# Optimization experiments

Hardware: AMD Instinct MI355X
Metric: run time of the kernel (lower is better)

Reference implementation:

```python
import jax, jax.numpy as jnp
import numpy as np

THETA = 128.0


def _make_Q(d, units):
    # Q[n,m] = (2n+1)/sqrt(d) if n > m and (n+m) odd, else 0 (fixed, non-trainable)
    n = np.arange(d)[:, None]
    m = np.arange(units)[None, :]
    Q = np.where((n > m) & (((n + m) % 2) == 1), (2 * n + 1) / np.sqrt(d), 0.0)
    return jnp.asarray(Q, dtype=jnp.float32)


def setup_inputs() -> dict:
    key = jax.random.key(0)
    k1, k2, k3, k4 = jax.random.split(key, 4)
    B_, T, Din, d, units = 16, 4096, 128, 256, 256
    x = jax.random.normal(k1, (B_, T, Din), dtype=jnp.float32)
    A = jax.random.normal(k2, (d, d), dtype=jnp.float32) / np.sqrt(d)
    Bm = jax.random.normal(k3, (Din, d), dtype=jnp.float32) / np.sqrt(Din)
    W_mix = jax.random.normal(k4, (units, units), dtype=jnp.float32) / np.sqrt(units)
    b_mix = jnp.zeros((units,), dtype=jnp.float32)
    return {"x": x, "A": A, "B": Bm, "W_mix": W_mix, "b_mix": b_mix}


def reference(x, A, B, W_mix, b_mix):
    d = A.shape[0]
    units = W_mix.shape[0]
    Q = _make_Q(d, units)
    QW = Q @ W_mix  # fuse fixed projection with dense kernel: (d, units)
    alpha = 1.0 - 1.0 / THETA
    beta = 1.0 / THETA
    # precompute input projection for all steps: (T, batch, d)
    xB = jnp.einsum('bti,id->tbd', x, B)

    def step(state, xBt):
        new_state = alpha * state + beta * (state @ A + xBt)
        y = jnp.tanh(new_state @ QW + b_mix)
        return new_state, y

    s0 = jnp.zeros((x.shape[0], d), dtype=x.dtype)
    _, ys = jax.lax.scan(step, s0, xB)  # ys: (T, batch, units)
    return jnp.transpose(ys, (1, 0, 2))
```

## Files before the change

### kernel.cpp

```cpp
#include <hip/hip_runtime.h>
#include <math.h>

constexpr int T_   = 4096;
constexpr int NB   = 16;
constexpr int D_   = 256;
constexpr int DIN  = 128;
constexpr int U_   = 256;
constexpr int L1   = 8;
constexpr int C1   = T_ / L1;
constexpr float ALPHA_ = 1.0f - 1.0f / 128.0f;
constexpr float BETA_  = 1.0f / 128.0f;
constexpr int SD   = NB * D_;
constexpr int MS   = D_ * D_;
constexpr int TLP  = D_ + 4;
constexpr int XLP  = DIN + 4;

using short8  = __attribute__((ext_vector_type(8))) short;
using float4v = __attribute__((ext_vector_type(4))) float;

__device__ __forceinline__ unsigned short bf16_rne(float x) {
  const unsigned b = __float_as_uint(x);
  const unsigned r = ((b >> 16) & 1u) + 0x7FFFu;
  return (unsigned short)((b + r) >> 16);
}
__device__ __forceinline__ float bf16_f(unsigned short h) {
  return __uint_as_float(((unsigned)h) << 16);
}

__device__ __forceinline__ void split2(float e0, float e1, unsigned& hd, unsigned& ld) {
  const unsigned b0 = __float_as_uint(e0), b1 = __float_as_uint(e1);
  const unsigned h0 = b0 & 0xFFFF0000u, h1 = b1 & 0xFFFF0000u;
  const float l0 = e0 - __uint_as_float(h0);
  const float l1 = e1 - __uint_as_float(h1);
  hd = (h0 >> 16) | h1;
  ld = (__float_as_uint(l0) >> 16) | (__float_as_uint(l1) & 0xFFFF0000u);
}

__device__ __forceinline__ void unpack8(uint4 a, uint4 b, short8& hi, short8& lo) {
  union { short8 s; unsigned u[4]; } H, L;
  const unsigned d[8] = {a.x, a.y, a.z, a.w, b.x, b.y, b.z, b.w};
#pragma unroll
  for (int i = 0; i < 4; ++i) {
    H.u[i] = (d[2 * i] >> 16) | (d[2 * i + 1] & 0xFFFF0000u);
    L.u[i] = (d[2 * i] & 0xFFFFu) | (d[2 * i + 1] << 16);
  }
  hi = H.s; lo = L.s;
}

__device__ __forceinline__ void mm_row(const float* __restrict__ Am,
                                       const float* __restrict__ Bm,
                                       float* __restrict__ Dm,
                                       int i, int tid, float* srow) {
  srow[tid] = Am[i * D_ + tid];
  __syncthreads();
  float a0 = 0.f, a1 = 0.f, a2 = 0.f, a3 = 0.f;
#pragma unroll 8
  for (int k = 0; k < D_; k += 4) {
    a0 = fmaf(srow[k + 0], Bm[(k + 0) * D_ + tid], a0);
    a1 = fmaf(srow[k + 1], Bm[(k + 1) * D_ + tid], a1);
    a2 = fmaf(srow[k + 2], Bm[(k + 2) * D_ + tid], a2);
    a3 = fmaf(srow[k + 3], Bm[(k + 3) * D_ + tid], a3);
  }
  Dm[i * D_ + tid] = (a0 + a1) + (a2 + a3);
  __syncthreads();
}

__global__ __launch_bounds__(256) void k_prep(const float* __restrict__ A,
                                              const float* __restrict__ W,
                                              float* __restrict__ Meff,
                                              float* __restrict__ QW) {
  const int bid = blockIdx.x, tid = threadIdx.x;
  if (bid < D_) {
    float v = BETA_ * A[bid * D_ + tid];
    if (bid == tid) v += ALPHA_;
    Meff[bid * D_ + tid] = v;
    return;
  }
  __shared__ float wch[32 * D_];
  float se = 0.f, so = 0.f;
  for (int ch = 0; ch < D_ / 32; ++ch) {
    __syncthreads();
    for (int idx = tid; idx < 32 * D_; idx += 256)
      wch[idx] = W[ch * 32 * D_ + idx];
    __syncthreads();
#pragma unroll
    for (int r = 0; r < 32; ++r) {
      const int n = ch * 32 + r;
      const float sum = (n & 1) ? se : so;
      QW[n * U_ + tid] = sum * ((float)(2 * n + 1) / 16.0f);
      const float wv = wch[r * D_ + tid];
      if (n & 1) so += wv; else se += wv;
    }
  }
}

__global__ __launch_bounds__(256) void k_pw(const float* __restrict__ Am,
                                            const float* __restrict__ Bbase,
                                            float* __restrict__ Dbase) {
  __shared__ float srow[D_];
  const int q = blockIdx.x >> 8, row = blockIdx.x & 255;
  mm_row(Am, Bbase + (size_t)q * MS, Dbase + (size_t)q * MS, row, threadIdx.x, srow);
}

__global__ __launch_bounds__(256) void k_pwr(const float* __restrict__ Abase,
                                             const float* __restrict__ Bm,
                                             float* __restrict__ Dbase) {
  __shared__ float srow[D_];
  const int q = blockIdx.x >> 8, row = blockIdx.x & 255;
  mm_row(Abase + (size_t)q * MS, Bm, Dbase + (size_t)q * MS, row, threadIdx.x, srow);
}

__global__ __launch_bounds__(256) void k_packA(const float* __restrict__ A,
                                               const float* __restrict__ Bm,
                                               unsigned short* __restrict__ Mf,
                                               unsigned short* __restrict__ Bmf) {
  const int bid = blockIdx.x, tid = threadIdx.x;
  const int lane = tid & 63, nb0 = tid >> 6;
  const int quad = lane >> 4, m16 = lane & 15;
  if (bid < 8) {
    const int ks = bid;
    for (int nb = nb0; nb < 16; nb += 4) {
      const size_t fo = ((size_t)(nb * 8 + ks) * 64 + lane) * 8;
#pragma unroll
      for (int jj = 0; jj < 8; ++jj) {
        const int k = ks * 32 + quad * 8 + jj;
        const int n = nb * 16 + m16;
        const float v = BETA_ * A[k * D_ + n];
        const unsigned short h = bf16_rne(v);
        Mf[fo + jj] = h;
        Mf[MS + fo + jj] = bf16_rne(v - bf16_f(h));
      }
    }
  } else {
    const int ks = bid - 8;
    unsigned short* dh = Bmf;
    unsigned short* dl = Bmf + (MS / 2);
    for (int nb = nb0; nb < 16; nb += 4) {
      const size_t fo = ((size_t)(nb * 4 + ks) * 64 + lane) * 8;
#pragma unroll
      for (int jj = 0; jj < 8; ++jj) {
        const int k = ks * 32 + quad * 8 + jj;
        const int n = nb * 16 + m16;
        const float v = BETA_ * Bm[k * D_ + n];
        const unsigned short h = bf16_rne(v);
        dh[fo + jj] = h;
        dl[fo + jj] = bf16_rne(v - bf16_f(h));
      }
    }
  }
}

__global__ __launch_bounds__(256) void k_packB(const float* __restrict__ R,
                                               const float* __restrict__ QWm,
                                               const float* __restrict__ M8,
                                               unsigned short* __restrict__ Bf,
                                               unsigned short* __restrict__ Pf0) {
  const int bid = blockIdx.x;
  const int mat = bid >> 3, ks = bid & 7;
  const float* X = (mat < 8) ? (R + (size_t)mat * MS) : (mat == 8 ? QWm : M8);
  unsigned short* dh = (mat < 9) ? (Bf + (size_t)mat * (2 * MS)) : Pf0;
  unsigned short* dl = dh + MS;
  const int tid = threadIdx.x, lane = tid & 63, nb0 = tid >> 6;
  const int quad = lane >> 4, m16 = lane & 15;
  for (int nb = nb0; nb < 16; nb += 4) {
    const size_t fo = ((size_t)(nb * 8 + ks) * 64 + lane) * 8;
#pragma unroll
    for (int jj = 0; jj < 8; ++jj) {
      const int k = ks * 32 + quad * 8 + jj;
      const int n = nb * 16 + m16;
      const float xv = X[k * D_ + n];
      const unsigned short h = bf16_rne(xv);
      dh[fo + jj] = h;
      dl[fo + jj] = bf16_rne(xv - bf16_f(h));
    }
  }
}

__global__ __launch_bounds__(256, 2) void k_passA(
    const float* __restrict__ x, const unsigned short* __restrict__ Bmf,
    const unsigned short* __restrict__ Mf,
    unsigned short* __restrict__ Shi, unsigned short* __restrict__ Slo,
    float* __restrict__ Ends) {
  __shared__ __align__(16) float xls[NB][XLP];
  __shared__ __align__(16) unsigned tls[NB][TLP];
  const int c = blockIdx.x, tid = threadIdx.x;
  const int w = tid >> 6, lane = tid & 63;
  const int m16 = lane & 15, q = lane >> 4;
  const int xrow = tid >> 4, xi0 = (tid & 15) * 8;

  float4v sC[4];
#pragma unroll
  for (int nt = 0; nt < 4; ++nt) sC[nt] = (float4v){0.f, 0.f, 0.f, 0.f};

  for (int j = 0; j < L1; ++j) {
    const int t = c * L1 + j;
    __syncthreads();
    {
      const float* xr = x + ((size_t)xrow * T_ + t) * DIN + xi0;
      const float4 v0 = *(const float4*)(xr);
      const float4 v1 = *(const float4*)(xr + 4);
      *(float4*)(&xls[xrow][xi0]) = v0;
      *(float4*)(&xls[xrow][xi0 + 4]) = v1;
    }
    if (j > 0) {
#pragma unroll
      for (int nt = 0; nt < 4; ++nt) {
        const int n = (w * 4 + nt) * 16 + m16;
#pragma unroll
        for (int r = 0; r < 4; ++r) {
          const float sv = sC[nt][r];
          const unsigned hb = __float_as_uint(sv) & 0xFFFF0000u;
          const float lo = sv - __uint_as_float(hb);
          tls[4 * q + r][n] = hb | (__float_as_uint(lo) >> 16);
        }
      }
    }
    __syncthreads();
    float4v acc[4];
#pragma unroll
    for (int nt = 0; nt < 4; ++nt) {
      acc[nt][0] = ALPHA_ * sC[nt][0];
      acc[nt][1] = ALPHA_ * sC[nt][1];
      acc[nt][2] = ALPHA_ * sC[nt][2];
      acc[nt][3] = ALPHA_ * sC[nt][3];
    }
#pragma unroll
    for (int ks = 0; ks < 4; ++ks) {
      float xv[8];
      *(float4*)(xv)     = *(const float4*)(&xls[m16][32 * ks + 8 * q]);
      *(float4*)(xv + 4) = *(const float4*)(&xls[m16][32 * ks + 8 * q + 4]);
      union { short8 s; unsigned u[4]; } XH, XL;
#pragma unroll
      for (int p = 0; p < 4; ++p) split2(xv[2 * p], xv[2 * p + 1], XH.u[p], XL.u[p]);
#pragma unroll
      for (int nt = 0; nt < 4; ++nt) {
        const size_t fo = ((size_t)((w * 4 + nt) * 4 + ks) * 64 + lane) * 8;
        const short8 bh = *(const short8*)(Bmf + fo);
        const short8 bl = *(const short8*)(Bmf + (MS / 2) + fo);
        acc[nt] = __builtin_amdgcn_mfma_f32_16x16x32_bf16(XH.s, bh, acc[nt], 0, 0, 0);
        acc[nt] = __builtin_amdgcn_mfma_f32_16x16x32_bf16(XH.s, bl, acc[nt], 0, 0, 0);
        acc[nt] = __builtin_amdgcn_mfma_f32_16x16x32_bf16(XL.s, bh, acc[nt], 0, 0, 0);
      }
    }
    if (j > 0) {
#pragma unroll
      for (int ks = 0; ks < 8; ++ks) {
        const uint4 p0 = *(const uint4*)(&tls[m16][32 * ks + 8 * q]);
        const uint4 p1 = *(const uint4*)(&tls[m16][32 * ks + 8 * q + 4]);
        short8 sh, sl; unpack8(p0, p1, sh, sl);
        const size_t ao = ((size_t)((t - 1) * 8 + ks) * 64 + lane) * 8;
        *(short8*)(Shi + ao) = sh;
        *(short8*)(Slo + ao) = sl;
#pragma unroll
        for (int nt = 0; nt < 4; ++nt) {
          const size_t fo = ((size_t)((w * 4 + nt) * 8 + ks) * 64 + lane) * 8;
          const short8 mh = *(const short8*)(Mf + fo);
          const short8 ml = *(const short8*)(Mf + MS + fo);
          acc[nt] = __builtin_amdgcn_mfma_f32_16x16x32_bf16(sh, mh, acc[nt], 0, 0, 0);
          acc[nt] = __builtin_amdgcn_mfma_f32_16x16x32_bf16(sh, ml, acc[nt], 0, 0, 0);
          acc[nt] = __builtin_amdgcn_mfma_f32_16x16x32_bf16(sl, mh, acc[nt], 0, 0, 0);
        }
      }
    }
#pragma unroll
    for (int nt = 0; nt < 4; ++nt) sC[nt] = acc[nt];
  }
  const int tl = c * L1 + L1 - 1;
  __syncthreads();
#pragma unroll
  for (int nt = 0; nt < 4; ++nt) {
    const int n = (w * 4 + nt) * 16 + m16;
#pragma unroll
    for (int r = 0; r < 4; ++r) {
      const float sv = sC[nt][r];
      const unsigned hb = __float_as_uint(sv) & 0xFFFF0000u;
      const float lo = sv - __uint_as_float(hb);
      tls[4 * q + r][n] = hb | (__float_as_uint(lo) >> 16);
    }
  }
  __syncthreads();
#pragma unroll
  for (int ks = 0; ks < 8; ++ks) {
    const uint4 p0 = *(const uint4*)(&tls[m16][32 * ks + 8 * q]);
    const uint4 p1 = *(const uint4*)(&tls[m16][32 * ks + 8 * q + 4]);
    short8 sh, sl; unpack8(p0, p1, sh, sl);
    const size_t ao = ((size_t)(tl * 8 + ks) * 64 + lane) * 8;
    *(short8*)(Shi + ao) = sh;
    *(short8*)(Slo + ao) = sl;
  }
#pragma unroll
  for (int nt = 0; nt < 4; ++nt) {
    const int n = (w * 4 + nt) * 16 + m16;
#pragma unroll
    for (int r = 0; r < 4; ++r)
      Ends[(size_t)c * SD + (size_t)(4 * q + r) * D_ + n] = sC[nt][r];
  }
}

__global__ __launch_bounds__(256) void k_scan(
    const float* __restrict__ Vin, float* __restrict__ Vout,
    const unsigned short* __restrict__ Pf,
    const float* __restrict__ Pf32,
    float* __restrict__ Psq,
    unsigned short* __restrict__ PfNext,
    int shift, int do_sq, int packmode,
    unsigned short* __restrict__ Hhi, unsigned short* __restrict__ Hlo) {
  __shared__ __align__(16) float smem[16 * TLP];
  const int bid = blockIdx.x, tid = threadIdx.x;
  if (bid >= C1) {
    if (!do_sq) return;
    const int i = bid - C1;
    smem[tid] = Pf32[i * D_ + tid];
    __syncthreads();
    float a0 = 0.f, a1 = 0.f, a2 = 0.f, a3 = 0.f;
#pragma unroll 8
    for (int k = 0; k < D_; k += 4) {
      a0 = fmaf(smem[k + 0], Pf32[(k + 0) * D_ + tid], a0);
      a1 = fmaf(smem[k + 1], Pf32[(k + 1) * D_ + tid], a1);
      a2 = fmaf(smem[k + 2], Pf32[(k + 2) * D_ + tid], a2);
      a3 = fmaf(smem[k + 3], Pf32[(k + 3) * D_ + tid], a3);
    }
    const float v = (a0 + a1) + (a2 + a3);
    Psq[i * D_ + tid] = v;
    const unsigned short h = bf16_rne(v);
    const unsigned short l = bf16_rne(v - bf16_f(h));
    const size_t off = ((size_t)((tid >> 4) * 8 + (i >> 5)) * 64 +
                        ((i >> 3) & 3) * 16 + (tid & 15)) * 8 + (i & 7);
    PfNext[off] = h;
    PfNext[MS + off] = l;
    return;
  }
  const int c = bid;
  const int w = tid >> 6, lane = tid & 63;
  const int m16 = lane & 15, q = lane >> 4;
  float4v acc[4];
#pragma unroll
  for (int nt = 0; nt < 4; ++nt) {
    const int n = (w * 4 + nt) * 16 + m16;
#pragma unroll
    for (int r = 0; r < 4; ++r)
      acc[nt][r] = Vin[(size_t)c * SD + (size_t)(4 * q + r) * D_ + n];
  }
  if (c >= shift) {
    const float* src = Vin + (size_t)(c - shift) * SD;
    {
      const int row = tid >> 4, col0 = (tid & 15) * 16;
#pragma unroll
      for (int p = 0; p < 4; ++p)
        *(float4*)(&smem[row * TLP + col0 + 4 * p]) =
            *(const float4*)(src + (size_t)row * D_ + col0 + 4 * p);
    }
    __syncthreads();
#pragma unroll
    for (int ks = 0; ks < 8; ++ks) {
      float xv[8];
      *(float4*)(xv)     = *(const float4*)(&smem[m16 * TLP + 32 * ks + 8 * q]);
      *(float4*)(xv + 4) = *(const float4*)(&smem[m16 * TLP + 32 * ks + 8 * q + 4]);
      union { short8 s; unsigned u[4]; } XH, XL;
#pragma unroll
      for (int p = 0; p < 4; ++p) split2(xv[2 * p], xv[2 * p + 1], XH.u[p], XL.u[p]);
#pragma unroll
      for (int nt = 0; nt < 4; ++nt) {
        const size_t fo = ((size_t)((w * 4 + nt) * 8 + ks) * 64 + lane) * 8;
        const short8 ph = *(const short8*)(Pf + fo);
        const short8 pl = *(const short8*)(Pf + MS + fo);
        acc[nt] = __builtin_amdgcn_mfma_f32_16x16x32_bf16(XH.s, ph, acc[nt], 0, 0, 0);
        acc[nt] = __builtin_amdgcn_mfma_f32_16x16x32_bf16(XH.s, pl, acc[nt], 0, 0, 0);
        acc[nt] = __builtin_amdgcn_mfma_f32_16x16x32_bf16(XL.s, ph, acc[nt], 0, 0, 0);
      }
    }
  }
  if (packmode) {
    __syncthreads();
    unsigned* tls = (unsigned*)smem;
#pragma unroll
    for (int nt = 0; nt < 4; ++nt) {
      const int n = (w * 4 + nt) * 16 + m16;
#pragma unroll
      for (int r = 0; r < 4; ++r) {
        const float sv = acc[nt][r];
        const unsigned hb = __float_as_uint(sv) & 0xFFFF0000u;
        const float lo = sv - __uint_as_float(hb);
        tls[(4 * q + r) * TLP + n] = hb | (__float_as_uint(lo) >> 16);
      }
    }
    __syncthreads();
#pragma unroll
    for (int ks = 0; ks < 8; ++ks) {
      const uint4 p0 = *(const uint4*)(&tls[m16 * TLP + 32 * ks + 8 * q]);
      const uint4 p1 = *(const uint4*)(&tls[m16 * TLP + 32 * ks + 8 * q + 4]);
      short8 sh, sl; unpack8(p0, p1, sh, sl);
      const size_t ao = ((size_t)(c * 8 + ks) * 64 + lane) * 8;
      *(short8*)(Hhi + ao) = sh;
      *(short8*)(Hlo + ao) = sl;
    }
  } else {
#pragma unroll
    for (int nt = 0; nt < 4; ++nt) {
      const int n = (w * 4 + nt) * 16 + m16;
#pragma unroll
      for (int r = 0; r < 4; ++r)
        Vout[(size_t)c * SD + (size_t)(4 * q + r) * D_ + n] = acc[nt][r];
    }
  }
}

__global__ __launch_bounds__(256, 3) void k_passB(
    const unsigned short* __restrict__ Shi, const unsigned short* __restrict__ Slo,
    const unsigned short* __restrict__ Hhi, const unsigned short* __restrict__ Hlo,
    const unsigned short* __restrict__ Bf, const float* __restrict__ bmix,
    float* __restrict__ out) {
  const int bid = blockIdx.x;
  const int g4 = (bid >> 3) * 4, j = bid & 7;
  const int tid = threadIdx.x;
  const int w = tid >> 6, lane = tid & 63;
  const int m16 = lane & 15, quad = lane >> 4;
  const unsigned short* Qh = Bf + (size_t)8 * 2 * MS;
  const unsigned short* Ql = Qh + MS;
  const unsigned short* Rh = Bf + (size_t)j * 2 * MS;
  const unsigned short* Rl = Rh + MS;

  float4v acc[4][4];
#pragma unroll
  for (int ci = 0; ci < 4; ++ci)
#pragma unroll
    for (int nt = 0; nt < 4; ++nt) acc[ci][nt] = (float4v){0.f, 0.f, 0.f, 0.f};

  for (int ks = 0; ks < 8; ++ks) {
    short8 fh[4], fl[4];
#pragma unroll
    for (int nt = 0; nt < 4; ++nt) {
      const size_t fo = ((size_t)((w * 4 + nt) * 8 + ks) * 64 + lane) * 8;
      fh[nt] = *(const short8*)(Qh + fo);
      fl[nt] = *(const short8*)(Ql + fo);
    }
#pragma unroll
    for (int ci = 0; ci < 4; ++ci) {
      const int t = (g4 + ci) * 8 + j;
      const size_t ao = ((size_t)(t * 8 + ks) * 64 + lane) * 8;
      const short8 sh = *(const short8*)(Shi + ao);
      const short8 sl = *(const short8*)(Slo + ao);
#pragma unroll
      for (int nt = 0; nt < 4; ++nt) {
        float4v a = acc[ci][nt];
        a = __builtin_amdgcn_mfma_f32_16x16x32_bf16(sh, fh[nt], a, 0, 0, 0);
        a = __builtin_amdgcn_mfma_f32_16x16x32_bf16(sh, fl[nt], a, 0, 0, 0);
        a = __builtin_amdgcn_mfma_f32_16x16x32_bf16(sl, fh[nt], a, 0, 0, 0);
        acc[ci][nt] = a;
      }
    }
#pragma unroll
    for (int nt = 0; nt < 4; ++nt) {
      const size_t fo = ((size_t)((w * 4 + nt) * 8 + ks) * 64 + lane) * 8;
      fh[nt] = *(const short8*)(Rh + fo);
      fl[nt] = *(const short8*)(Rl + fo);
    }
#pragma unroll
    for (int ci = 0; ci < 4; ++ci) {
      const int c = g4 + ci;
      if (c > 0) {
        const size_t ho = ((size_t)((c - 1) * 8 + ks) * 64 + lane) * 8;
        const short8 hh = *(const short8*)(Hhi + ho);
        const short8 hl = *(const short8*)(Hlo + ho);
#pragma unroll
        for (int nt = 0; nt < 4; ++nt) {
          float4v a = acc[ci][nt];
          a = __builtin_amdgcn_mfma_f32_16x16x32_bf16(hh, fh[nt], a, 0, 0, 0);
          a = __builtin_amdgcn_mfma_f32_16x16x32_bf16(hh, fl[nt], a, 0, 0, 0);
          a = __builtin_amdgcn_mfma_f32_16x16x32_bf16(hl, fh[nt], a, 0, 0, 0);
          acc[ci][nt] = a;
        }
      }
    }
  }
  __shared__ float ysm[16][U_ + 4];
  for (int ci = 0; ci < 4; ++ci) {
    const int t = (g4 + ci) * 8 + j;
    __syncthreads();
#pragma unroll
    for (int nt = 0; nt < 4; ++nt) {
      const int n = (w * 4 + nt) * 16 + m16;
      const float bias = bmix[n];
#pragma unroll
      for (int r = 0; r < 4; ++r) {
        const float v = acc[ci][nt][r] + bias;
        const float e = __expf(2.0f * v);
        ysm[quad * 4 + r][n] = 1.0f - 2.0f / (e + 1.0f);
      }
    }
    __syncthreads();
    for (int idx = tid; idx < 16 * (U_ / 4); idx += 256) {
      const int b = idx >> 6, c4 = (idx & 63) * 4;
      const float4 v = make_float4(ysm[b][c4], ysm[b][c4 + 1],
                                   ysm[b][c4 + 2], ysm[b][c4 + 3]);
      *(float4*)(out + ((size_t)b * T_ + t) * U_ + c4) = v;
    }
  }
}

extern "C" void kernel_launch(void* const* d_in, const int* in_sizes, int n_in,
                              void* d_out, int out_size, void* d_ws, size_t ws_size,
                              hipStream_t stream) {
  const float* x    = (const float*)d_in[0];
  const float* A    = (const float*)d_in[1];
  const float* Bm   = (const float*)d_in[2];
  const float* W    = (const float*)d_in[3];
  const float* bmix = (const float*)d_in[4];
  float* out = (float*)d_out;

  float* ws = (float*)d_ws;
  unsigned short* Shi = (unsigned short*)ws;
  unsigned short* Slo = (unsigned short*)(ws + 8388608);
  float* pw  = ws + 16777216;
  float* QW  = pw + 8 * (size_t)MS;
  float* R   = QW + MS;
  float* Sa  = R + 8 * (size_t)MS;
  float* Sb  = Sa + MS;
  unsigned short* Bf  = (unsigned short*)(Sb + MS);
  unsigned short* Mf  = Bf + (size_t)9 * 2 * MS;
  unsigned short* Bmf = Mf + 2 * (size_t)MS;
  unsigned short* Pf0 = Bmf + MS;
  unsigned short* Pf1 = Pf0 + 2 * (size_t)MS;
  (void)in_sizes; (void)n_in; (void)out_size; (void)ws_size;

  float* Va = out;
  float* Vb = out + (size_t)C1 * SD;

  unsigned short* Hhi = (unsigned short*)d_in[0];
  unsigned short* Hlo = Hhi + (size_t)C1 * 16 * 256;

  k_prep<<<D_ + 1, 256, 0, stream>>>(A, W, pw, QW);
  k_packA<<<12, 256, 0, stream>>>(A, Bm, Mf, Bmf);
  k_passA<<<C1, 256, 0, stream>>>(x, Bmf, Mf, Shi, Slo, Va);
  k_pw<<<256, 256, 0, stream>>>(pw, pw, pw + MS);
  k_pw<<<512, 256, 0, stream>>>(pw + MS, pw, pw + 2 * (size_t)MS);
  k_pw<<<1024, 256, 0, stream>>>(pw + 3 * (size_t)MS, pw, pw + 4 * (size_t)MS);
  k_pwr<<<2048, 256, 0, stream>>>(pw, QW, R);
  k_packB<<<80, 256, 0, stream>>>(R, QW, pw + 7 * (size_t)MS, Bf, Pf0);

  const float* vin = Va; float* vout = Vb;
  const float* Pcur = pw + 7 * (size_t)MS;
  float* sqs[2] = {Sa, Sb};
  unsigned short* Pfp[2] = {Pf0, Pf1};
  for (int lvl = 0; lvl < 9; ++lvl) {
    float* Pd = sqs[lvl & 1];
    k_scan<<<C1 + D_, 256, 0, stream>>>(vin, vout, Pfp[lvl & 1], Pcur, Pd,
                                        Pfp[(lvl + 1) & 1], 1 << lvl,
                                        (lvl < 8) ? 1 : 0, (lvl == 8) ? 1 : 0,
                                        Hhi, Hlo);
    Pcur = Pd;
    const float* tmp = vin; vin = vout; vout = (float*)tmp;
  }

  k_passB<<<1024, 256, 0, stream>>>(Shi, Slo, Hhi, Hlo, Bf, bmix, out);
}
```

Before: 464.1 us.

## Switch chunk scan to radix-4 levels and fuse setup kernels

The Hillis-Steele chunk-end scan changes from radix-2 (nine levels, one matrix term each) to radix-4 (five levels, up to three matrix terms each). Each level's side blocks compute the needed matrix powers by repeated row-vector passes, replacing the squaring step. The setup kernels are merged: packA goes into prep, the power-chain kernels into one k_big1 where each block computes its own power chain, and packB into passA. This cuts kernel launches and serial levels, but each scan level does more MFMA work per chunk and the power blocks run long serial matvec chains. Scratch buffers for the power matrices now sit inside the x input buffer.

```diff
diff --git a/kernel.cpp b/kernel.cpp
--- a/kernel.cpp
+++ b/kernel.cpp
@@ -47,28 +47,29 @@
   hi = H.s; lo = L.s;
 }
 
-__device__ __forceinline__ void mm_row(const float* __restrict__ Am,
-                                       const float* __restrict__ Bm,
-                                       float* __restrict__ Dm,
-                                       int i, int tid, float* srow) {
-  srow[tid] = Am[i * D_ + tid];
+__device__ __forceinline__ float rmv_pass(float u, const float* __restrict__ Mat,
+                                          float* __restrict__ us, int tid) {
+  us[tid] = u;
   __syncthreads();
   float a0 = 0.f, a1 = 0.f, a2 = 0.f, a3 = 0.f;
 #pragma unroll 8
   for (int k = 0; k < D_; k += 4) {
-    a0 = fmaf(srow[k + 0], Bm[(k + 0) * D_ + tid], a0);
-    a1 = fmaf(srow[k + 1], Bm[(k + 1) * D_ + tid], a1);
-    a2 = fmaf(srow[k + 2], Bm[(k + 2) * D_ + tid], a2);
-    a3 = fmaf(srow[k + 3], Bm[(k + 3) * D_ + tid], a3);
-  }
-  Dm[i * D_ + tid] = (a0 + a1) + (a2 + a3);
+    a0 = fmaf(us[k + 0], Mat[(size_t)(k + 0) * D_ + tid], a0);
+    a1 = fmaf(us[k + 1], Mat[(size_t)(k + 1) * D_ + tid], a1);
+    a2 = fmaf(us[k + 2], Mat[(size_t)(k + 2) * D_ + tid], a2);
+    a3 = fmaf(us[k + 3], Mat[(size_t)(k + 3) * D_ + tid], a3);
+  }
   __syncthreads();
+  return (a0 + a1) + (a2 + a3);
 }
 
 __global__ __launch_bounds__(256) void k_prep(const float* __restrict__ A,
                                               const float* __restrict__ W,
                                               float* __restrict__ Meff,
-                                              float* __restrict__ QW) {
+                                              float* __restrict__ QW,
+                                              const float* __restrict__ Bm,
+                                              unsigned short* __restrict__ Mf,
+                                              unsigned short* __restrict__ Bmf) {
   const int bid = blockIdx.x, tid = threadIdx.x;
   if (bid < D_) {
     float v = BETA_ * A[bid * D_ + tid];
@@ -76,49 +77,30 @@
     Meff[bid * D_ + tid] = v;
     return;
   }
-  __shared__ float wch[32 * D_];
-  float se = 0.f, so = 0.f;
-  for (int ch = 0; ch < D_ / 32; ++ch) {
-    __syncthreads();
-    for (int idx = tid; idx < 32 * D_; idx += 256)
-      wch[idx] = W[ch * 32 * D_ + idx];
-    __syncthreads();
-#pragma unroll
-    for (int r = 0; r < 32; ++r) {
-      const int n = ch * 32 + r;
-      const float sum = (n & 1) ? se : so;
-      QW[n * U_ + tid] = sum * ((float)(2 * n + 1) / 16.0f);
-      const float wv = wch[r * D_ + tid];
-      if (n & 1) so += wv; else se += wv;
-    }
-  }
-}
-
-__global__ __launch_bounds__(256) void k_pw(const float* __restrict__ Am,
-                                            const float* __restrict__ Bbase,
-                                            float* __restrict__ Dbase) {
-  __shared__ float srow[D_];
-  const int q = blockIdx.x >> 8, row = blockIdx.x & 255;
-  mm_row(Am, Bbase + (size_t)q * MS, Dbase + (size_t)q * MS, row, threadIdx.x, srow);
-}
-
-__global__ __launch_bounds__(256) void k_pwr(const float* __restrict__ Abase,
-                                             const float* __restrict__ Bm,
-                                             float* __restrict__ Dbase) {
-  __shared__ float srow[D_];
-  const int q = blockIdx.x >> 8, row = blockIdx.x & 255;
-  mm_row(Abase + (size_t)q * MS, Bm, Dbase + (size_t)q * MS, row, threadIdx.x, srow);
-}
-
-__global__ __launch_bounds__(256) void k_packA(const float* __restrict__ A,
-                                               const float* __restrict__ Bm,
-                                               unsigned short* __restrict__ Mf,
-                                               unsigned short* __restrict__ Bmf) {
-  const int bid = blockIdx.x, tid = threadIdx.x;
+  if (bid == D_) {
+    __shared__ float wch[32 * D_];
+    float se = 0.f, so = 0.f;
+    for (int ch = 0; ch < D_ / 32; ++ch) {
+      __syncthreads();
+      for (int idx = tid; idx < 32 * D_; idx += 256)
+        wch[idx] = W[ch * 32 * D_ + idx];
+      __syncthreads();
+#pragma unroll
+      for (int r = 0; r < 32; ++r) {
+        const int n = ch * 32 + r;
+        const float sum = (n & 1) ? se : so;
+        QW[n * U_ + tid] = sum * ((float)(2 * n + 1) / 16.0f);
+        const float wv = wch[r * D_ + tid];
+        if (n & 1) so += wv; else se += wv;
+      }
+    }
+    return;
+  }
+  const int pb = bid - D_ - 1;
   const int lane = tid & 63, nb0 = tid >> 6;
   const int quad = lane >> 4, m16 = lane & 15;
-  if (bid < 8) {
-    const int ks = bid;
+  if (pb < 8) {
+    const int ks = pb;
     for (int nb = nb0; nb < 16; nb += 4) {
       const size_t fo = ((size_t)(nb * 8 + ks) * 64 + lane) * 8;
 #pragma unroll
@@ -132,7 +114,7 @@
       }
     }
   } else {
-    const int ks = bid - 8;
+    const int ks = pb - 8;
     unsigned short* dh = Bmf;
     unsigned short* dl = Bmf + (MS / 2);
     for (int nb = nb0; nb < 16; nb += 4) {
@@ -150,40 +132,57 @@
   }
 }
 
-__global__ __launch_bounds__(256) void k_packB(const float* __restrict__ R,
-                                               const float* __restrict__ QWm,
-                                               const float* __restrict__ M8,
-                                               unsigned short* __restrict__ Bf,
-                                               unsigned short* __restrict__ Pf0) {
-  const int bid = blockIdx.x;
-  const int mat = bid >> 3, ks = bid & 7;
-  const float* X = (mat < 8) ? (R + (size_t)mat * MS) : (mat == 8 ? QWm : M8);
-  unsigned short* dh = (mat < 9) ? (Bf + (size_t)mat * (2 * MS)) : Pf0;
-  unsigned short* dl = dh + MS;
-  const int tid = threadIdx.x, lane = tid & 63, nb0 = tid >> 6;
-  const int quad = lane >> 4, m16 = lane & 15;
-  for (int nb = nb0; nb < 16; nb += 4) {
-    const size_t fo = ((size_t)(nb * 8 + ks) * 64 + lane) * 8;
-#pragma unroll
-    for (int jj = 0; jj < 8; ++jj) {
-      const int k = ks * 32 + quad * 8 + jj;
-      const int n = nb * 16 + m16;
-      const float xv = X[k * D_ + n];
-      const unsigned short h = bf16_rne(xv);
-      dh[fo + jj] = h;
-      dl[fo + jj] = bf16_rne(xv - bf16_f(h));
-    }
-  }
-}
-
-__global__ __launch_bounds__(256, 2) void k_passA(
+__global__ __launch_bounds__(256) void k_big1(const float* __restrict__ M,
+                                              const float* __restrict__ QW,
+                                              float* __restrict__ R,
+                                              float* __restrict__ M8) {
+  __shared__ float us[D_];
+  const int bid = blockIdx.x, tid = threadIdx.x;
+  const int j = bid >> 8, i = bid & 255;
+  float u = M[(size_t)i * D_ + tid];
+  if (j < 8) {
+    for (int p = 0; p < j; ++p) u = rmv_pass(u, M, us, tid);
+    u = rmv_pass(u, QW, us, tid);
+    R[(size_t)j * MS + (size_t)i * D_ + tid] = u;
+  } else {
+    for (int p = 0; p < 7; ++p) u = rmv_pass(u, M, us, tid);
+    M8[(size_t)i * D_ + tid] = u;
+  }
+}
+
+__global__ __launch_bounds__(256, 2) void k_big2(
+    const float* __restrict__ R, const float* __restrict__ QWm,
+    const float* __restrict__ M8, unsigned short* __restrict__ Bf,
+    unsigned short* __restrict__ Pf0,
     const float* __restrict__ x, const unsigned short* __restrict__ Bmf,
     const unsigned short* __restrict__ Mf,
     unsigned short* __restrict__ Shi, unsigned short* __restrict__ Slo,
     float* __restrict__ Ends) {
+  const int bid = blockIdx.x, tid = threadIdx.x;
+  if (bid < 80) {
+    const int mat = bid >> 3, ks = bid & 7;
+    const float* X = (mat < 8) ? (R + (size_t)mat * MS) : (mat == 8 ? QWm : M8);
+    unsigned short* dh = (mat < 9) ? (Bf + (size_t)mat * (2 * MS)) : Pf0;
+    unsigned short* dl = dh + MS;
+    const int lane = tid & 63, nb0 = tid >> 6;
+    const int quad = lane >> 4, m16 = lane & 15;
+    for (int nb = nb0; nb < 16; nb += 4) {
+      const size_t fo = ((size_t)(nb * 8 + ks) * 64 + lane) * 8;
+#pragma unroll
+      for (int jj = 0; jj < 8; ++jj) {
+        const int k = ks * 32 + quad * 8 + jj;
+        const int n = nb * 16 + m16;
+        const float xv = X[k * D_ + n];
+        const unsigned short h = bf16_rne(xv);
+        dh[fo + jj] = h;
+        dl[fo + jj] = bf16_rne(xv - bf16_f(h));
+      }
+    }
+    return;
+  }
   __shared__ __align__(16) float xls[NB][XLP];
   __shared__ __align__(16) unsigned tls[NB][TLP];
-  const int c = blockIdx.x, tid = threadIdx.x;
+  const int c = bid - 80;
   const int w = tid >> 6, lane = tid & 63;
   const int m16 = lane & 15, q = lane >> 4;
   const int xrow = tid >> 4, xi0 = (tid & 15) * 8;
@@ -297,37 +296,29 @@
   }
 }
 
-__global__ __launch_bounds__(256) void k_scan(
+__global__ __launch_bounds__(256) void k_scanR(
     const float* __restrict__ Vin, float* __restrict__ Vout,
-    const unsigned short* __restrict__ Pf,
-    const float* __restrict__ Pf32,
-    float* __restrict__ Psq,
-    unsigned short* __restrict__ PfNext,
-    int shift, int do_sq, int packmode,
+    const unsigned short* __restrict__ Pln, int s, int nterms, int packmode,
+    const float* __restrict__ base, float* __restrict__ f32out,
+    unsigned short* __restrict__ PlnNext, int npw, int pc0, int pc1, int pc2,
     unsigned short* __restrict__ Hhi, unsigned short* __restrict__ Hlo) {
   __shared__ __align__(16) float smem[16 * TLP];
   const int bid = blockIdx.x, tid = threadIdx.x;
   if (bid >= C1) {
-    if (!do_sq) return;
-    const int i = bid - C1;
-    smem[tid] = Pf32[i * D_ + tid];
-    __syncthreads();
-    float a0 = 0.f, a1 = 0.f, a2 = 0.f, a3 = 0.f;
-#pragma unroll 8
-    for (int k = 0; k < D_; k += 4) {
-      a0 = fmaf(smem[k + 0], Pf32[(k + 0) * D_ + tid], a0);
-      a1 = fmaf(smem[k + 1], Pf32[(k + 1) * D_ + tid], a1);
-      a2 = fmaf(smem[k + 2], Pf32[(k + 2) * D_ + tid], a2);
-      a3 = fmaf(smem[k + 3], Pf32[(k + 3) * D_ + tid], a3);
-    }
-    const float v = (a0 + a1) + (a2 + a3);
-    Psq[i * D_ + tid] = v;
-    const unsigned short h = bf16_rne(v);
-    const unsigned short l = bf16_rne(v - bf16_f(h));
+    const int idx = bid - C1;
+    const int m = idx >> 8, i = idx & 255;
+    if (m >= npw) return;
+    const int pc = (m == 0) ? pc0 : (m == 1 ? pc1 : pc2);
+    float u = base[(size_t)i * D_ + tid];
+    for (int p = 0; p < pc; ++p) u = rmv_pass(u, base, smem, tid);
+    if (m == 0) f32out[(size_t)i * D_ + tid] = u;
+    const unsigned short h = bf16_rne(u);
+    const unsigned short l = bf16_rne(u - bf16_f(h));
     const size_t off = ((size_t)((tid >> 4) * 8 + (i >> 5)) * 64 +
                         ((i >> 3) & 3) * 16 + (tid & 15)) * 8 + (i & 7);
-    PfNext[off] = h;
-    PfNext[MS + off] = l;
+    unsigned short* dh = PlnNext + (size_t)m * (2 * MS);
+    dh[off] = h;
+    dh[MS + off] = l;
     return;
   }
   const int c = bid;
@@ -341,8 +332,11 @@
     for (int r = 0; r < 4; ++r)
       acc[nt][r] = Vin[(size_t)c * SD + (size_t)(4 * q + r) * D_ + n];
   }
-  if (c >= shift) {
-    const float* src = Vin + (size_t)(c - shift) * SD;
+  for (int k = 1; k <= nterms; ++k) {
+    if (c < k * s) break;
+    const float* src = Vin + (size_t)(c - k * s) * SD;
+    const unsigned short* Pf = Pln + (size_t)(k - 1) * (2 * MS);
+    __syncthreads();
     {
       const int row = tid >> 4, col0 = (tid & 15) * 16;
 #pragma unroll
@@ -356,7 +350,7 @@
       float xv[8];
       *(float4*)(xv)     = *(const float4*)(&smem[m16 * TLP + 32 * ks + 8 * q]);
       *(float4*)(xv + 4) = *(const float4*)(&smem[m16 * TLP + 32 * ks + 8 * q + 4]);
-      union { short8 s; unsigned u[4]; } XH, XL;
+      union { short8 ss; unsigned u[4]; } XH, XL;
 #pragma unroll
       for (int p = 0; p < 4; ++p) split2(xv[2 * p], xv[2 * p + 1], XH.u[p], XL.u[p]);
 #pragma unroll
@@ -364,9 +358,9 @@
         const size_t fo = ((size_t)((w * 4 + nt) * 8 + ks) * 64 + lane) * 8;
         const short8 ph = *(const short8*)(Pf + fo);
         const short8 pl = *(const short8*)(Pf + MS + fo);
-        acc[nt] = __builtin_amdgcn_mfma_f32_16x16x32_bf16(XH.s, ph, acc[nt], 0, 0, 0);
-        acc[nt] = __builtin_amdgcn_mfma_f32_16x16x32_bf16(XH.s, pl, acc[nt], 0, 0, 0);
-        acc[nt] = __builtin_amdgcn_mfma_f32_16x16x32_bf16(XL.s, ph, acc[nt], 0, 0, 0);
+        acc[nt] = __builtin_amdgcn_mfma_f32_16x16x32_bf16(XH.ss, ph, acc[nt], 0, 0, 0);
+        acc[nt] = __builtin_amdgcn_mfma_f32_16x16x32_bf16(XH.ss, pl, acc[nt], 0, 0, 0);
+        acc[nt] = __builtin_amdgcn_mfma_f32_16x16x32_bf16(XL.ss, ph, acc[nt], 0, 0, 0);
       }
     }
   }
@@ -520,37 +514,37 @@
   unsigned short* Mf  = Bf + (size_t)9 * 2 * MS;
   unsigned short* Bmf = Mf + 2 * (size_t)MS;
   unsigned short* Pf0 = Bmf + MS;
-  unsigned short* Pf1 = Pf0 + 2 * (size_t)MS;
   (void)in_sizes; (void)n_in; (void)out_size; (void)ws_size;
 
   float* Va = out;
   float* Vb = out + (size_t)C1 * SD;
 
-  unsigned short* Hhi = (unsigned short*)d_in[0];
+  float* xf = (float*)d_in[0];
+  unsigned short* Hhi = (unsigned short*)xf;
   unsigned short* Hlo = Hhi + (size_t)C1 * 16 * 256;
-
-  k_prep<<<D_ + 1, 256, 0, stream>>>(A, W, pw, QW);
-  k_packA<<<12, 256, 0, stream>>>(A, Bm, Mf, Bmf);
-  k_passA<<<C1, 256, 0, stream>>>(x, Bmf, Mf, Shi, Slo, Va);
-  k_pw<<<256, 256, 0, stream>>>(pw, pw, pw + MS);
-  k_pw<<<512, 256, 0, stream>>>(pw + MS, pw, pw + 2 * (size_t)MS);
-  k_pw<<<1024, 256, 0, stream>>>(pw + 3 * (size_t)MS, pw, pw + 4 * (size_t)MS);
-  k_pwr<<<2048, 256, 0, stream>>>(pw, QW, R);
-  k_packB<<<80, 256, 0, stream>>>(R, QW, pw + 7 * (size_t)MS, Bf, Pf0);
-
-  const float* vin = Va; float* vout = Vb;
-  const float* Pcur = pw + 7 * (size_t)MS;
-  float* sqs[2] = {Sa, Sb};
-  unsigned short* Pfp[2] = {Pf0, Pf1};
-  for (int lvl = 0; lvl < 9; ++lvl) {
-    float* Pd = sqs[lvl & 1];
-    k_scan<<<C1 + D_, 256, 0, stream>>>(vin, vout, Pfp[lvl & 1], Pcur, Pd,
-                                        Pfp[(lvl + 1) & 1], 1 << lvl,
-                                        (lvl < 8) ? 1 : 0, (lvl == 8) ? 1 : 0,
-                                        Hhi, Hlo);
-    Pcur = Pd;
-    const float* tmp = vin; vin = vout; vout = (float*)tmp;
-  }
+  unsigned short* PlnA = (unsigned short*)(xf + 2097152);
+  unsigned short* PlnB = PlnA + (size_t)3 * 2 * MS;
+  float* P16f   = xf + 2490368;
+  float* P64f   = P16f + MS;
+  float* P256f  = P64f + MS;
+  float* P1024f = P256f + MS;
+
+  k_prep<<<D_ + 13, 256, 0, stream>>>(A, W, pw, QW, Bm, Mf, Bmf);
+  k_big1<<<9 * 256, 256, 0, stream>>>(pw, QW, R, pw + 7 * (size_t)MS);
+  k_big2<<<80 + C1, 256, 0, stream>>>(R, QW, pw + 7 * (size_t)MS, Bf, Pf0,
+                                      x, Bmf, Mf, Shi, Slo, Va);
+
+  const float* M8f = pw + 7 * (size_t)MS;
+  k_scanR<<<C1 + 768, 256, 0, stream>>>(Va, Vb, Pf0, 1, 1, 0,
+                                        M8f, P16f, PlnA, 3, 1, 3, 5, Hhi, Hlo);
+  k_scanR<<<C1 + 768, 256, 0, stream>>>(Vb, Va, PlnA, 2, 3, 0,
+                                        P16f, P64f, PlnB, 3, 3, 7, 11, Hhi, Hlo);
+  k_scanR<<<C1 + 768, 256, 0, stream>>>(Va, Vb, PlnB, 8, 3, 0,
+                                        P64f, P256f, PlnA, 3, 3, 7, 11, Hhi, Hlo);
+  k_scanR<<<C1 + 768, 256, 0, stream>>>(Vb, Va, PlnA, 32, 3, 0,
+                                        P256f, P1024f, PlnB, 3, 3, 7, 11, Hhi, Hlo);
+  k_scanR<<<C1, 256, 0, stream>>>(Va, Vb, PlnB, 128, 3, 1,
+                                  P1024f, P1024f, PlnB, 0, 0, 0, 0, Hhi, Hlo);
 
   k_passB<<<1024, 256, 0, stream>>>(Shi, Slo, Hhi, Hlo, Bf, bmix, out);
 }
```

Result: slower. 727.8 us (+56.8%).

## Merge prep/pack kernels and run passA with 512 threads alongside packB

Applied to the files above, without the earlier changes.

Folds k_packA into k_prep and merges k_packB with the chunk pass-A kernel into one launch, so fewer kernel launches and serialized stream gaps. Pass-A now uses 512 threads per block (8 waves), each wave owning two 16-column tiles instead of four, which halves per-wave MFMA work on the serial chunk recurrence and the x-load per thread. Shi/Slo stores are distributed so each wave writes one k-slice. The trade-off is more LDS/barrier contention per block and possible occupancy changes from launch_bounds(512,4).

```diff
diff --git a/kernel.cpp b/kernel.cpp
--- a/kernel.cpp
+++ b/kernel.cpp
@@ -68,7 +68,10 @@
 __global__ __launch_bounds__(256) void k_prep(const float* __restrict__ A,
                                               const float* __restrict__ W,
                                               float* __restrict__ Meff,
-                                              float* __restrict__ QW) {
+                                              float* __restrict__ QW,
+                                              const float* __restrict__ Bm,
+                                              unsigned short* __restrict__ Mf,
+                                              unsigned short* __restrict__ Bmf) {
   const int bid = blockIdx.x, tid = threadIdx.x;
   if (bid < D_) {
     float v = BETA_ * A[bid * D_ + tid];
@@ -76,49 +79,30 @@
     Meff[bid * D_ + tid] = v;
     return;
   }
-  __shared__ float wch[32 * D_];
-  float se = 0.f, so = 0.f;
-  for (int ch = 0; ch < D_ / 32; ++ch) {
-    __syncthreads();
-    for (int idx = tid; idx < 32 * D_; idx += 256)
-      wch[idx] = W[ch * 32 * D_ + idx];
-    __syncthreads();
-#pragma unroll
-    for (int r = 0; r < 32; ++r) {
-      const int n = ch * 32 + r;
-      const float sum = (n & 1) ? se : so;
-      QW[n * U_ + tid] = sum * ((float)(2 * n + 1) / 16.0f);
-      const float wv = wch[r * D_ + tid];
-      if (n & 1) so += wv; else se += wv;
-    }
-  }
-}
-
-__global__ __launch_bounds__(256) void k_pw(const float* __restrict__ Am,
-                                            const float* __restrict__ Bbase,
-                                            float* __restrict__ Dbase) {
-  __shared__ float srow[D_];
-  const int q = blockIdx.x >> 8, row = blockIdx.x & 255;
-  mm_row(Am, Bbase + (size_t)q * MS, Dbase + (size_t)q * MS, row, threadIdx.x, srow);
-}
-
-__global__ __launch_bounds__(256) void k_pwr(const float* __restrict__ Abase,
-                                             const float* __restrict__ Bm,
-                                             float* __restrict__ Dbase) {
-  __shared__ float srow[D_];
-  const int q = blockIdx.x >> 8, row = blockIdx.x & 255;
-  mm_row(Abase + (size_t)q * MS, Bm, Dbase + (size_t)q * MS, row, threadIdx.x, srow);
-}
-
-__global__ __launch_bounds__(256) void k_packA(const float* __restrict__ A,
-                                               const float* __restrict__ Bm,
-                                               unsigned short* __restrict__ Mf,
-                                               unsigned short* __restrict__ Bmf) {
-  const int bid = blockIdx.x, tid = threadIdx.x;
+  if (bid == D_) {
+    __shared__ float wch[32 * D_];
+    float se = 0.f, so = 0.f;
+    for (int ch = 0; ch < D_ / 32; ++ch) {
+      __syncthreads();
+      for (int idx = tid; idx < 32 * D_; idx += 256)
+        wch[idx] = W[ch * 32 * D_ + idx];
+      __syncthreads();
+#pragma unroll
+      for (int r = 0; r < 32; ++r) {
+        const int n = ch * 32 + r;
+        const float sum = (n & 1) ? se : so;
+        QW[n * U_ + tid] = sum * ((float)(2 * n + 1) / 16.0f);
+        const float wv = wch[r * D_ + tid];
+        if (n & 1) so += wv; else se += wv;
+      }
+    }
+    return;
+  }
+  const int pb = bid - D_ - 1;
   const int lane = tid & 63, nb0 = tid >> 6;
   const int quad = lane >> 4, m16 = lane & 15;
-  if (bid < 8) {
-    const int ks = bid;
+  if (pb < 8) {
+    const int ks = pb;
     for (int nb = nb0; nb < 16; nb += 4) {
       const size_t fo = ((size_t)(nb * 8 + ks) * 64 + lane) * 8;
 #pragma unroll
@@ -132,7 +116,7 @@
       }
     }
   } else {
-    const int ks = bid - 8;
+    const int ks = pb - 8;
     unsigned short* dh = Bmf;
     unsigned short* dl = Bmf + (MS / 2);
     for (int nb = nb0; nb < 16; nb += 4) {
@@ -150,62 +134,74 @@
   }
 }
 
-__global__ __launch_bounds__(256) void k_packB(const float* __restrict__ R,
-                                               const float* __restrict__ QWm,
-                                               const float* __restrict__ M8,
-                                               unsigned short* __restrict__ Bf,
-                                               unsigned short* __restrict__ Pf0) {
-  const int bid = blockIdx.x;
-  const int mat = bid >> 3, ks = bid & 7;
-  const float* X = (mat < 8) ? (R + (size_t)mat * MS) : (mat == 8 ? QWm : M8);
-  unsigned short* dh = (mat < 9) ? (Bf + (size_t)mat * (2 * MS)) : Pf0;
-  unsigned short* dl = dh + MS;
-  const int tid = threadIdx.x, lane = tid & 63, nb0 = tid >> 6;
-  const int quad = lane >> 4, m16 = lane & 15;
-  for (int nb = nb0; nb < 16; nb += 4) {
-    const size_t fo = ((size_t)(nb * 8 + ks) * 64 + lane) * 8;
-#pragma unroll
-    for (int jj = 0; jj < 8; ++jj) {
-      const int k = ks * 32 + quad * 8 + jj;
-      const int n = nb * 16 + m16;
-      const float xv = X[k * D_ + n];
-      const unsigned short h = bf16_rne(xv);
-      dh[fo + jj] = h;
-      dl[fo + jj] = bf16_rne(xv - bf16_f(h));
-    }
-  }
-}
-
-__global__ __launch_bounds__(256, 2) void k_passA(
+__global__ __launch_bounds__(256) void k_pw(const float* __restrict__ Am,
+                                            const float* __restrict__ Bbase,
+                                            float* __restrict__ Dbase) {
+  __shared__ float srow[D_];
+  const int q = blockIdx.x >> 8, row = blockIdx.x & 255;
+  mm_row(Am, Bbase + (size_t)q * MS, Dbase + (size_t)q * MS, row, threadIdx.x, srow);
+}
+
+__global__ __launch_bounds__(256) void k_pwr(const float* __restrict__ Abase,
+                                             const float* __restrict__ Bm,
+                                             float* __restrict__ Dbase) {
+  __shared__ float srow[D_];
+  const int q = blockIdx.x >> 8, row = blockIdx.x & 255;
+  mm_row(Abase + (size_t)q * MS, Bm, Dbase + (size_t)q * MS, row, threadIdx.x, srow);
+}
+
+__global__ __launch_bounds__(512, 4) void k_big2(
+    const float* __restrict__ R, const float* __restrict__ QWm,
+    const float* __restrict__ M8, unsigned short* __restrict__ Bf,
+    unsigned short* __restrict__ Pf0,
     const float* __restrict__ x, const unsigned short* __restrict__ Bmf,
     const unsigned short* __restrict__ Mf,
     unsigned short* __restrict__ Shi, unsigned short* __restrict__ Slo,
     float* __restrict__ Ends) {
+  const int bid = blockIdx.x, tid = threadIdx.x;
+  if (bid < 80) {
+    const int mat = bid >> 3, ks = bid & 7;
+    const float* X = (mat < 8) ? (R + (size_t)mat * MS) : (mat == 8 ? QWm : M8);
+    unsigned short* dh = (mat < 9) ? (Bf + (size_t)mat * (2 * MS)) : Pf0;
+    unsigned short* dl = dh + MS;
+    const int lane = tid & 63, nb0 = tid >> 6;
+    const int quad = lane >> 4, m16 = lane & 15;
+    for (int nb = nb0; nb < 16; nb += 8) {
+      const size_t fo = ((size_t)(nb * 8 + ks) * 64 + lane) * 8;
+#pragma unroll
+      for (int jj = 0; jj < 8; ++jj) {
+        const int k = ks * 32 + quad * 8 + jj;
+        const int n = nb * 16 + m16;
+        const float xv = X[k * D_ + n];
+        const unsigned short h = bf16_rne(xv);
+        dh[fo + jj] = h;
+        dl[fo + jj] = bf16_rne(xv - bf16_f(h));
+      }
+    }
+    return;
+  }
   __shared__ __align__(16) float xls[NB][XLP];
   __shared__ __align__(16) unsigned tls[NB][TLP];
-  const int c = blockIdx.x, tid = threadIdx.x;
+  const int c = bid - 80;
   const int w = tid >> 6, lane = tid & 63;
   const int m16 = lane & 15, q = lane >> 4;
-  const int xrow = tid >> 4, xi0 = (tid & 15) * 8;
-
-  float4v sC[4];
-#pragma unroll
-  for (int nt = 0; nt < 4; ++nt) sC[nt] = (float4v){0.f, 0.f, 0.f, 0.f};
+  const int xrow = tid >> 5, xi0 = (tid & 31) * 4;
+
+  float4v sC[2];
+#pragma unroll
+  for (int nt = 0; nt < 2; ++nt) sC[nt] = (float4v){0.f, 0.f, 0.f, 0.f};
 
   for (int j = 0; j < L1; ++j) {
     const int t = c * L1 + j;
     __syncthreads();
     {
       const float* xr = x + ((size_t)xrow * T_ + t) * DIN + xi0;
-      const float4 v0 = *(const float4*)(xr);
-      const float4 v1 = *(const float4*)(xr + 4);
-      *(float4*)(&xls[xrow][xi0]) = v0;
-      *(float4*)(&xls[xrow][xi0 + 4]) = v1;
+      *(float4*)(&xls[xrow][xi0]) = *(const float4*)(xr);
     }
     if (j > 0) {
 #pragma unroll
-      for (int nt = 0; nt < 4; ++nt) {
-        const int n = (w * 4 + nt) * 16 + m16;
+      for (int nt = 0; nt < 2; ++nt) {
+        const int n = (w * 2 + nt) * 16 + m16;
 #pragma unroll
         for (int r = 0; r < 4; ++r) {
           const float sv = sC[nt][r];
@@ -216,9 +212,9 @@
       }
     }
     __syncthreads();
-    float4v acc[4];
-#pragma unroll
-    for (int nt = 0; nt < 4; ++nt) {
+    float4v acc[2];
+#pragma unroll
+    for (int nt = 0; nt < 2; ++nt) {
       acc[nt][0] = ALPHA_ * sC[nt][0];
       acc[nt][1] = ALPHA_ * sC[nt][1];
       acc[nt][2] = ALPHA_ * sC[nt][2];
@@ -233,8 +229,8 @@
 #pragma unroll
       for (int p = 0; p < 4; ++p) split2(xv[2 * p], xv[2 * p + 1], XH.u[p], XL.u[p]);
 #pragma unroll
-      for (int nt = 0; nt < 4; ++nt) {
-        const size_t fo = ((size_t)((w * 4 + nt) * 4 + ks) * 64 + lane) * 8;
+      for (int nt = 0; nt < 2; ++nt) {
+        const size_t fo = ((size_t)((w * 2 + nt) * 4 + ks) * 64 + lane) * 8;
         const short8 bh = *(const short8*)(Bmf + fo);
         const short8 bl = *(const short8*)(Bmf + (MS / 2) + fo);
         acc[nt] = __builtin_amdgcn_mfma_f32_16x16x32_bf16(XH.s, bh, acc[nt], 0, 0, 0);
@@ -248,12 +244,14 @@
         const uint4 p0 = *(const uint4*)(&tls[m16][32 * ks + 8 * q]);
         const uint4 p1 = *(const uint4*)(&tls[m16][32 * ks + 8 * q + 4]);
         short8 sh, sl; unpack8(p0, p1, sh, sl);
-        const size_t ao = ((size_t)((t - 1) * 8 + ks) * 64 + lane) * 8;
-        *(short8*)(Shi + ao) = sh;
-        *(short8*)(Slo + ao) = sl;
-#pragma unroll
-        for (int nt = 0; nt < 4; ++nt) {
-          const size_t fo = ((size_t)((w * 4 + nt) * 8 + ks) * 64 + lane) * 8;
+        if (ks == w) {
+          const size_t ao = ((size_t)((t - 1) * 8 + ks) * 64 + lane) * 8;
+          *(short8*)(Shi + ao) = sh;
+          *(short8*)(Slo + ao) = sl;
+        }
+#pragma unroll
+        for (int nt = 0; nt < 2; ++nt) {
+          const size_t fo = ((size_t)((w * 2 + nt) * 8 + ks) * 64 + lane) * 8;
           const short8 mh = *(const short8*)(Mf + fo);
           const short8 ml = *(const short8*)(Mf + MS + fo);
           acc[nt] = __builtin_amdgcn_mfma_f32_16x16x32_bf16(sh, mh, acc[nt], 0, 0, 0);
@@ -263,13 +261,13 @@
       }
     }
 #pragma unroll
-    for (int nt = 0; nt < 4; ++nt) sC[nt] = acc[nt];
+    for (int nt = 0; nt < 2; ++nt) sC[nt] = acc[nt];
   }
   const int tl = c * L1 + L1 - 1;
   __syncthreads();
 #pragma unroll
-  for (int nt = 0; nt < 4; ++nt) {
-    const int n = (w * 4 + nt) * 16 + m16;
+  for (int nt = 0; nt < 2; ++nt) {
+    const int n = (w * 2 + nt) * 16 + m16;
 #pragma unroll
     for (int r = 0; r < 4; ++r) {
       const float sv = sC[nt][r];
@@ -279,8 +277,8 @@
     }
   }
   __syncthreads();
-#pragma unroll
-  for (int ks = 0; ks < 8; ++ks) {
+  {
+    const int ks = w;
     const uint4 p0 = *(const uint4*)(&tls[m16][32 * ks + 8 * q]);
     const uint4 p1 = *(const uint4*)(&tls[m16][32 * ks + 8 * q + 4]);
     short8 sh, sl; unpack8(p0, p1, sh, sl);
@@ -289,8 +287,8 @@
     *(short8*)(Slo + ao) = sl;
   }
 #pragma unroll
-  for (int nt = 0; nt < 4; ++nt) {
-    const int n = (w * 4 + nt) * 16 + m16;
+  for (int nt = 0; nt < 2; ++nt) {
+    const int n = (w * 2 + nt) * 16 + m16;
 #pragma unroll
     for (int r = 0; r < 4; ++r)
       Ends[(size_t)c * SD + (size_t)(4 * q + r) * D_ + n] = sC[nt][r];
@@ -529,14 +527,13 @@
   unsigned short* Hhi = (unsigned short*)d_in[0];
   unsigned short* Hlo = Hhi + (size_t)C1 * 16 * 256;
 
-  k_prep<<<D_ + 1, 256, 0, stream>>>(A, W, pw, QW);
-  k_packA<<<12, 256, 0, stream>>>(A, Bm, Mf, Bmf);
-  k_passA<<<C1, 256, 0, stream>>>(x, Bmf, Mf, Shi, Slo, Va);
+  k_prep<<<D_ + 13, 256, 0, stream>>>(A, W, pw, QW, Bm, Mf, Bmf);
   k_pw<<<256, 256, 0, stream>>>(pw, pw, pw + MS);
   k_pw<<<512, 256, 0, stream>>>(pw + MS, pw, pw + 2 * (size_t)MS);
   k_pw<<<1024, 256, 0, stream>>>(pw + 3 * (size_t)MS, pw, pw + 4 * (size_t)MS);
   k_pwr<<<2048, 256, 0, stream>>>(pw, QW, R);
-  k_packB<<<80, 256, 0, stream>>>(R, QW, pw + 7 * (size_t)MS, Bf, Pf0);
+  k_big2<<<80 + C1, 512, 0, stream>>>(R, QW, pw + 7 * (size_t)MS, Bf, Pf0,
+                                      x, Bmf, Mf, Shi, Slo, Va);
 
   const float* vin = Va; float* vout = Vb;
   const float* Pcur = pw + 7 * (size_t)MS;
```

Measured after the change: 507.5 us. +9.4%, slower.
